# Kernel optimization log

Hardware: AMD Instinct MI355X
Metric: run time of the kernel (lower is better)

Reference implementation:

```python
import jax, jax.numpy as jnp
import numpy as np

EPS = 1e-8
NUM_HEADS = 4


def setup_inputs() -> dict:
    key = jax.random.key(0)
    ks = jax.random.split(key, 20)
    N, D = 8192, 200      # total nodes, gnn/text dim
    B = 4                  # graphs (text batch)
    E, DEG = 4096, 16      # hyperedges, nodes per hyperedge
    H = 128                # fusion hidden dim
    f = lambda k, s: jax.random.normal(k, s, dtype=jnp.float32) * 0.05
    return {
        "x": jax.random.normal(ks[0], (N, D), dtype=jnp.float32),
        "text": jax.random.normal(ks[1], (B, D), dtype=jnp.float32),
        "W": f(ks[2], (D, D)),
        "b": jnp.zeros((D,), jnp.float32),
        "gate_w": f(ks[3], (D, 1)),
        "gate_b": jnp.zeros((1,), jnp.float32),
        "gnn_w": f(ks[4], (D, H)), "gnn_b": f(ks[5], (H,)),
        "text_w": f(ks[6], (D, H)), "text_b": f(ks[7], (H,)),
        "in_w": f(ks[8], (H, 3 * H)), "in_b": f(ks[9], (3 * H,)),
        "attn_out_w": f(ks[10], (H, H)), "attn_out_b": f(ks[11], (H,)),
        "fgate_w": f(ks[12], (2 * H, H)), "fgate_b": f(ks[13], (H,)),
        "outp_w": f(ks[14], (H, D)), "outp_b": f(ks[15], (D,)),
        "edge_nodes": jax.random.randint(ks[16], (E, DEG), 0, N),
    }


def _forward(x, text, W, b, gate_w, gate_b, gnn_w, gnn_b, text_w, text_b,
             in_w, in_b, attn_out_w, attn_out_b, fgate_w, fgate_b,
             outp_w, outp_b, edge_nodes):
    N, D = x.shape
    E, DEG = edge_nodes.shape
    # --- HypergraphConv: incidence build + normalized Laplacian propagation ---
    out = x @ W                                         # [N, D]
    # H[node, edge] = 1/len(edge); duplicates overwrite (set), as in torch loop
    Hinc = jnp.zeros((N, E), x.dtype).at[edge_nodes, jnp.arange(E)[:, None]].set(1.0 / DEG)
    Dv = Hinc.sum(axis=1)                               # node degree [N]
    De = Hinc.sum(axis=0)                               # edge degree [E]
    dv = 1.0 / jnp.sqrt(Dv + EPS)
    de = 1.0 / (De + EPS)
    Hl = Hinc * dv[:, None]                             # Dv^-1/2 H
    L = (Hl * de[None, :]) @ Hl.T                       # Dv^-1/2 H De^-1 H^T Dv^-1/2
    hyper_out = L @ out                                 # [N, D]
    alpha = jax.nn.sigmoid(x.mean(axis=0, keepdims=True) @ gate_w + gate_b)  # [1,1]
    gnn_feat = alpha * out + (1.0 - alpha) * hyper_out + b
    # --- CrossModalAttentionFusion on per-graph node features (3D path) ---
    B = text.shape[0]
    Nn = N // B
    gnn3 = gnn_feat.reshape(B, Nn, D)
    gp = gnn3 @ gnn_w + gnn_b                           # [B, Nn, H]
    tp = (text @ text_w + text_b)[:, None, :]           # [B, 1, H]
    Hd = gp.shape[-1]
    hd = Hd // NUM_HEADS
    q = gp @ in_w[:, :Hd] + in_b[:Hd]
    k = tp @ in_w[:, Hd:2 * Hd] + in_b[Hd:2 * Hd]
    v = tp @ in_w[:, 2 * Hd:] + in_b[2 * Hd:]
    qh = q.reshape(B, Nn, NUM_HEADS, hd).transpose(0, 2, 1, 3)   # [B,h,Nn,hd]
    kh = k.reshape(B, 1, NUM_HEADS, hd).transpose(0, 2, 1, 3)    # [B,h,1,hd]
    vh = v.reshape(B, 1, NUM_HEADS, hd).transpose(0, 2, 1, 3)
    scores = jnp.einsum("bhqd,bhkd->bhqk", qh, kh) / jnp.sqrt(jnp.float32(hd))
    attn = jax.nn.softmax(scores, axis=-1)              # kv_len=1 -> ones
    att = jnp.einsum("bhqk,bhkd->bhqd", attn, vh)
    att = att.transpose(0, 2, 1, 3).reshape(B, Nn, Hd) @ attn_out_w + attn_out_b
    g = jax.nn.sigmoid(jnp.concatenate([gp, att], axis=-1) @ fgate_w + fgate_b)
    fused = g * gp + (1.0 - g) * att
    return fused @ outp_w + outp_b                      # [B, Nn, D]


def reference(x, text, W, b, gate_w, gate_b, gnn_w, gnn_b, text_w, text_b,
              in_w, in_b, attn_out_w, attn_out_b, fgate_w, fgate_b,
              outp_w, outp_b, edge_nodes):
    return _forward(x, text, W, b, gate_w, gate_b, gnn_w, gnn_b, text_w, text_b,
                    in_w, in_b, attn_out_w, attn_out_b, fgate_w, fgate_b,
                    outp_w, outp_b, edge_nodes)
```

## Files before the change

kernel.cpp:

```cpp
#include <hip/hip_runtime.h>
#include <hip/hip_bf16.h>

#define NODES 8192
#define DIM   200
#define NEDGE 4096
#define DEGREE 16
#define NB    4
#define NNODE 2048
#define HD    128
#define MT    8
#define ECAP  64

__global__ void k_front(const float* __restrict__ x, const int* __restrict__ en,
                        const float* __restrict__ W, const float* __restrict__ gnn_w,
                        const float* __restrict__ bias, const float* __restrict__ gnn_b,
                        const float* __restrict__ text, const float* __restrict__ text_w,
                        const float* __restrict__ text_b, const float* __restrict__ in_w,
                        const float* __restrict__ in_b, const float* __restrict__ aow,
                        const float* __restrict__ aob, const float* __restrict__ fgw,
                        const float* __restrict__ fgb, float* __restrict__ colsum,
                        int* __restrict__ cnt, int* __restrict__ emask,
                        float* __restrict__ Wg, float* __restrict__ bg,
                        float* __restrict__ attO, float* __restrict__ attg) {
    __shared__ float st[DIM];
    __shared__ float part[2][HD];
    __shared__ float vin[HD];
    int b = blockIdx.x, t = threadIdx.x;
    if (b < 256) {
        if (t < DIM) {
            float acc = 0.f;
            int r0 = b * 32;
            for (int r = 0; r < 32; r++) acc += x[(r0 + r) * DIM + t];
            atomicAdd(&colsum[t], acc);
        }
        return;
    }
    if (b < 272) {
        int e = (b - 256) * 256 + t;
        int idx[DEGREE];
#pragma unroll
        for (int i = 0; i < DEGREE; i++) idx[i] = en[e * DEGREE + i];
        int mask = 0;
#pragma unroll
        for (int i = 0; i < DEGREE; i++) {
            bool uniq = true;
            for (int j = 0; j < i; j++) uniq = uniq && (idx[j] != idx[i]);
            if (uniq) { mask |= (1 << i); atomicAdd(&cnt[idx[i]], 1); }
        }
        emask[e] = mask;
        return;
    }
    if (b < 372) {
        int r = 2 * (b - 272) + (t >> 7);
        int c = t & 127;
        const float* vec = &W[r * DIM];
        float acc = 0.f;
        for (int k = 0; k < DIM; k++) acc += vec[k] * gnn_w[k * HD + c];
        Wg[r * HD + c] = acc;
        return;
    }
    if (b == 372) {
        if (t < HD) {
            float acc = 0.f;
            for (int k = 0; k < DIM; k++) acc += bias[k] * gnn_w[k * HD + t];
            bg[t] = acc + gnn_b[t];
        }
        return;
    }
    int g = b - 373;
    int c = t & 127, h = t >> 7;
    if (t < DIM) st[t] = text[g * DIM + t];
    __syncthreads();
    {
        float acc = 0.f;
        int k0 = h * 100;
        for (int k = k0; k < k0 + 100; k++) acc += st[k] * text_w[k * HD + c];
        part[h][c] = acc;
    }
    __syncthreads();
    if (t < HD) vin[t] = part[0][t] + part[1][t] + text_b[t];
    __syncthreads();
    {
        float acc = 0.f;
        int k0 = h * 64;
        for (int k = k0; k < k0 + 64; k++) acc += vin[k] * in_w[k * 3 * HD + 2 * HD + c];
        part[h][c] = acc;
    }
    __syncthreads();
    if (t < HD) vin[t] = part[0][t] + part[1][t] + in_b[2 * HD + t];
    __syncthreads();
    {
        float acc = 0.f;
        int k0 = h * 64;
        for (int k = k0; k < k0 + 64; k++) acc += vin[k] * aow[k * HD + c];
        part[h][c] = acc;
    }
    __syncthreads();
    if (t < HD) {
        float ao = part[0][t] + part[1][t] + aob[t];
        attO[g * HD + t] = ao;
        vin[t] = ao;
    }
    __syncthreads();
    {
        float acc = 0.f;
        int k0 = h * 64;
        for (int k = k0; k < k0 + 64; k++) acc += vin[k] * fgw[(HD + k) * HD + c];
        part[h][c] = acc;
    }
    __syncthreads();
    if (t < HD) attg[g * HD + t] = part[0][t] + part[1][t] + fgb[t];
}

__global__ void k_mid(const float* __restrict__ colsum, const float* __restrict__ gate_w,
                      const float* __restrict__ gate_b, float* __restrict__ alpha,
                      const int* __restrict__ cnt, int* __restrict__ off,
                      int* __restrict__ cursor, float* __restrict__ dv) {
    __shared__ float redf[1024];
    __shared__ int wsum[16];
    int t = threadIdx.x;
    if (blockIdx.x == 0) {
        redf[t] = (t < DIM) ? colsum[t] * gate_w[t] : 0.f;
        __syncthreads();
        for (int o = 512; o > 0; o >>= 1) {
            if (t < o) redf[t] += redf[t + o];
            __syncthreads();
        }
        if (t == 0) {
            float z = redf[0] / (float)NODES + gate_b[0];
            alpha[0] = 1.0f / (1.0f + expf(-z));
        }
        return;
    }
    int base = t * 8;
    int local[8];
    int s = 0;
#pragma unroll
    for (int i = 0; i < 8; i++) { local[i] = cnt[base + i]; s += local[i]; }
    int lane = t & 63, wv = t >> 6;
    int v = s;
    for (int d = 1; d < 64; d <<= 1) {
        int u = __shfl_up(v, d);
        if (lane >= d) v += u;
    }
    if (lane == 63) wsum[wv] = v;
    __syncthreads();
    if (t == 0) {
        int run = 0;
        for (int i = 0; i < 16; i++) { int tmp = wsum[i]; wsum[i] = run; run += tmp; }
    }
    __syncthreads();
    int run = wsum[wv] + v - s;
#pragma unroll
    for (int i = 0; i < 8; i++) {
        off[base + i] = run;
        cursor[base + i] = run;
        dv[base + i] = 1.0f / sqrtf((float)local[i] * (1.0f / 16.0f) + 1e-8f);
        run += local[i];
    }
    if (t == 1023) off[NODES] = run;
}

__global__ void k_xwgfill(const float* __restrict__ x, const float* __restrict__ Wg,
                          float* __restrict__ out2, const int* __restrict__ en,
                          const int* __restrict__ emask, int* __restrict__ cursor,
                          int* __restrict__ elist) {
    __shared__ float sx[MT][DIM];
    int t = threadIdx.x;
    if (blockIdx.x >= NODES / MT) {
        int e = (blockIdx.x - NODES / MT) * 256 + t;
        int m = emask[e];
#pragma unroll
        for (int i = 0; i < DEGREE; i++) {
            if ((m >> i) & 1) {
                int n = en[e * DEGREE + i];
                int p = atomicAdd(&cursor[n], 1);
                elist[p] = e;
            }
        }
        return;
    }
    int bm = blockIdx.x * MT;
    for (int i = t; i < MT * DIM; i += 256) sx[i / DIM][i % DIM] = x[bm * DIM + i];
    __syncthreads();
    int c = t & 127, rg = t >> 7;
    float acc[4] = {0.f, 0.f, 0.f, 0.f};
    for (int k = 0; k < DIM; k++) {
        float w = Wg[k * HD + c];
#pragma unroll
        for (int i = 0; i < 4; i++) acc[i] += sx[rg * 4 + i][k] * w;
    }
#pragma unroll
    for (int i = 0; i < 4; i++) out2[(bm + rg * 4 + i) * HD + c] = acc[i];
}

__global__ void k_tE(const int* __restrict__ en, const int* __restrict__ emask,
                     const float* __restrict__ dv, const float* __restrict__ out2,
                     float* __restrict__ tE) {
    int e = blockIdx.x * 2 + (threadIdx.x >> 7);
    int c = threadIdx.x & 127;
    int m = emask[e];
    float De = (float)__popc(m) * (1.0f / 16.0f);
    float de = 1.0f / (De + 1e-8f);
    float acc = 0.f;
#pragma unroll
    for (int i = 0; i < DEGREE; i++) {
        if ((m >> i) & 1) {
            int nd = en[e * DEGREE + i];
            acc += dv[nd] * out2[nd * HD + c];
        }
    }
    tE[e * HD + c] = de * acc;
}

__global__ void k_tail(const float* __restrict__ out2, const float* __restrict__ tE,
                       const float* __restrict__ dv, const int* __restrict__ off,
                       const int* __restrict__ elist, const float* __restrict__ alpha,
                       const float* __restrict__ bg, const float* __restrict__ fgw,
                       const float* __restrict__ attO, const float* __restrict__ attg,
                       const float* __restrict__ opw, const float* __restrict__ opb,
                       float* __restrict__ out) {
    __shared__ float sgp[MT][HD];
    __shared__ int   sl[MT][ECAP];
    __shared__ int   scount[MT];
    int bm = blockIdx.x * MT;
    int b = bm >> 11;
    int t = threadIdx.x;
    {
        int r = t >> 5, l = t & 31;
        int n = bm + r;
        int j0 = off[n], j1 = off[n + 1];
        int cc = j1 - j0;
        if (l == 0) scount[r] = cc;
        int lim = cc < ECAP ? cc : ECAP;
        for (int j = l; j < lim; j += 32) sl[r][j] = elist[j0 + j];
    }
    __syncthreads();
    int c = t & 127, rg = t >> 7;
    float a = alpha[0];
    float bgc = bg[c];
#pragma unroll
    for (int i = 0; i < 4; i++) {
        int r = rg * 4 + i;
        int n = bm + r;
        int cc = scount[r];
        int lim = cc < ECAP ? cc : ECAP;
        float hyp = 0.f;
        for (int j = 0; j < lim; j++) hyp += tE[sl[r][j] * HD + c];
        if (cc > ECAP) {
            int j0 = off[n];
            for (int j = ECAP; j < cc; j++) hyp += tE[elist[j0 + j] * HD + c];
        }
        hyp *= dv[n] * (1.0f / 256.0f);
        sgp[r][c] = a * out2[n * HD + c] + (1.0f - a) * hyp + bgc;
    }
    __syncthreads();
    float ao = attO[b * HD + c];
    float ag = attg[b * HD + c];
    float acc[4] = {ag, ag, ag, ag};
    for (int j = 0; j < HD; j++) {
        float w = fgw[j * HD + c];
#pragma unroll
        for (int i = 0; i < 4; i++) acc[i] += sgp[rg * 4 + i][j] * w;
    }
    __syncthreads();
#pragma unroll
    for (int i = 0; i < 4; i++) {
        int r = rg * 4 + i;
        float g = 1.0f / (1.0f + expf(-acc[i]));
        sgp[r][c] = g * sgp[r][c] + (1.0f - g) * ao;
    }
    __syncthreads();
    if (t < DIM) {
        float accO[MT];
        float ob = opb[t];
#pragma unroll
        for (int i = 0; i < MT; i++) accO[i] = ob;
        for (int j = 0; j < HD; j++) {
            float w = opw[j * DIM + t];
#pragma unroll
            for (int i = 0; i < MT; i++) accO[i] += sgp[i][j] * w;
        }
#pragma unroll
        for (int i = 0; i < MT; i++) out[(bm + i) * DIM + t] = accO[i];
    }
}

extern "C" void kernel_launch(void* const* d_in, const int* in_sizes, int n_in,
                              void* d_out, int out_size, void* d_ws, size_t ws_size,
                              hipStream_t stream) {
    const float* x      = (const float*)d_in[0];
    const float* text   = (const float*)d_in[1];
    const float* W      = (const float*)d_in[2];
    const float* bias   = (const float*)d_in[3];
    const float* gate_w = (const float*)d_in[4];
    const float* gate_b = (const float*)d_in[5];
    const float* gnn_w  = (const float*)d_in[6];
    const float* gnn_b  = (const float*)d_in[7];
    const float* text_w = (const float*)d_in[8];
    const float* text_b = (const float*)d_in[9];
    const float* in_w   = (const float*)d_in[10];
    const float* in_b   = (const float*)d_in[11];
    const float* aow    = (const float*)d_in[12];
    const float* aob    = (const float*)d_in[13];
    const float* fgw    = (const float*)d_in[14];
    const float* fgb    = (const float*)d_in[15];
    const float* opw    = (const float*)d_in[16];
    const float* opb    = (const float*)d_in[17];
    const int*   en     = (const int*)d_in[18];
    float* out = (float*)d_out;

    char* p = (char*)d_ws;
    int*   cnt    = (int*)p;   p += NODES * sizeof(int);
    float* colsum = (float*)p; p += DIM * sizeof(float);
    float* out2   = (float*)p; p += (size_t)NODES * HD * sizeof(float);
    float* tE     = (float*)p; p += (size_t)NEDGE * HD * sizeof(float);
    float* Wg     = (float*)p; p += DIM * HD * sizeof(float);
    float* dv     = (float*)p; p += NODES * sizeof(float);
    float* alpha  = (float*)p; p += sizeof(float);
    float* bg     = (float*)p; p += HD * sizeof(float);
    float* attO   = (float*)p; p += NB * HD * sizeof(float);
    float* attg   = (float*)p; p += NB * HD * sizeof(float);
    int*   off    = (int*)p;   p += (NODES + 1) * sizeof(int);
    int*   cursor = (int*)p;   p += NODES * sizeof(int);
    int*   emask  = (int*)p;   p += NEDGE * sizeof(int);
    int*   elist  = (int*)p;   p += (size_t)NEDGE * DEGREE * sizeof(int);

    hipMemsetAsync(cnt, 0, (NODES + DIM) * sizeof(int), stream);

    k_front<<<377, 256, 0, stream>>>(x, en, W, gnn_w, bias, gnn_b, text, text_w,
                                     text_b, in_w, in_b, aow, aob, fgw, fgb,
                                     colsum, cnt, emask, Wg, bg, attO, attg);
    k_mid<<<2, 1024, 0, stream>>>(colsum, gate_w, gate_b, alpha, cnt, off, cursor, dv);
    k_xwgfill<<<NODES / MT + 16, 256, 0, stream>>>(x, Wg, out2, en, emask, cursor, elist);
    k_tE<<<NEDGE / 2, 256, 0, stream>>>(en, emask, dv, out2, tE);
    k_tail<<<NODES / MT, 256, 0, stream>>>(out2, tE, dv, off, elist, alpha, bg, fgw,
                                           attO, attg, opw, opb, out);
}
```

Measured before the change: 173.9 us.

## Replace CSR node-to-edge gather with atomic scatter from hyperedges

Drops the prefix-scan kernel and the CSR edge-list build. Each hyperedge block now computes its aggregated value and atomically adds it into a per-node accumulator, instead of the tail kernel gathering tE through the edge list. This removes one kernel launch, the per-node atomic cursor fill and the indirect gather. In exchange it adds a large memset of the accumulator, float atomics with nondeterministic summation order, and the dv computation is folded into the projection kernel as extra blocks. The x tile is now loaded into shared memory with float4.

```diff
diff --git a/kernel.cpp b/kernel.cpp
--- a/kernel.cpp
+++ b/kernel.cpp
@@ -9,7 +9,6 @@
 #define NNODE 2048
 #define HD    128
 #define MT    8
-#define ECAP  64
 
 __global__ void k_front(const float* __restrict__ x, const int* __restrict__ en,
                         const float* __restrict__ W, const float* __restrict__ gnn_w,
@@ -112,130 +111,79 @@
     if (t < HD) attg[g * HD + t] = part[0][t] + part[1][t] + fgb[t];
 }
 
-__global__ void k_mid(const float* __restrict__ colsum, const float* __restrict__ gate_w,
-                      const float* __restrict__ gate_b, float* __restrict__ alpha,
-                      const int* __restrict__ cnt, int* __restrict__ off,
-                      int* __restrict__ cursor, float* __restrict__ dv) {
-    __shared__ float redf[1024];
-    __shared__ int wsum[16];
+__global__ void k_xwg(const float* __restrict__ x, const float* __restrict__ Wg,
+                      float* __restrict__ out2, const float* __restrict__ colsum,
+                      const float* __restrict__ gate_w, const float* __restrict__ gate_b,
+                      float* __restrict__ alpha, const int* __restrict__ cnt,
+                      float* __restrict__ dv) {
+    __shared__ float sx[MT * DIM];
     int t = threadIdx.x;
-    if (blockIdx.x == 0) {
-        redf[t] = (t < DIM) ? colsum[t] * gate_w[t] : 0.f;
+    if (blockIdx.x == NODES / MT) {
+        __shared__ float red[256];
+        red[t] = (t < DIM) ? colsum[t] * gate_w[t] : 0.f;
         __syncthreads();
-        for (int o = 512; o > 0; o >>= 1) {
-            if (t < o) redf[t] += redf[t + o];
+        for (int o = 128; o > 0; o >>= 1) {
+            if (t < o) red[t] += red[t + o];
             __syncthreads();
         }
         if (t == 0) {
-            float z = redf[0] / (float)NODES + gate_b[0];
+            float z = red[0] / (float)NODES + gate_b[0];
             alpha[0] = 1.0f / (1.0f + expf(-z));
         }
         return;
     }
-    int base = t * 8;
-    int local[8];
-    int s = 0;
-#pragma unroll
-    for (int i = 0; i < 8; i++) { local[i] = cnt[base + i]; s += local[i]; }
-    int lane = t & 63, wv = t >> 6;
-    int v = s;
-    for (int d = 1; d < 64; d <<= 1) {
-        int u = __shfl_up(v, d);
-        if (lane >= d) v += u;
-    }
-    if (lane == 63) wsum[wv] = v;
-    __syncthreads();
-    if (t == 0) {
-        int run = 0;
-        for (int i = 0; i < 16; i++) { int tmp = wsum[i]; wsum[i] = run; run += tmp; }
-    }
-    __syncthreads();
-    int run = wsum[wv] + v - s;
-#pragma unroll
-    for (int i = 0; i < 8; i++) {
-        off[base + i] = run;
-        cursor[base + i] = run;
-        dv[base + i] = 1.0f / sqrtf((float)local[i] * (1.0f / 16.0f) + 1e-8f);
-        run += local[i];
-    }
-    if (t == 1023) off[NODES] = run;
-}
-
-__global__ void k_xwgfill(const float* __restrict__ x, const float* __restrict__ Wg,
-                          float* __restrict__ out2, const int* __restrict__ en,
-                          const int* __restrict__ emask, int* __restrict__ cursor,
-                          int* __restrict__ elist) {
-    __shared__ float sx[MT][DIM];
-    int t = threadIdx.x;
-    if (blockIdx.x >= NODES / MT) {
-        int e = (blockIdx.x - NODES / MT) * 256 + t;
-        int m = emask[e];
-#pragma unroll
-        for (int i = 0; i < DEGREE; i++) {
-            if ((m >> i) & 1) {
-                int n = en[e * DEGREE + i];
-                int p = atomicAdd(&cursor[n], 1);
-                elist[p] = e;
-            }
-        }
+    if (blockIdx.x > NODES / MT) {
+        int n = (blockIdx.x - NODES / MT - 1) * 256 + t;
+        dv[n] = 1.0f / sqrtf((float)cnt[n] * (1.0f / 16.0f) + 1e-8f);
         return;
     }
     int bm = blockIdx.x * MT;
-    for (int i = t; i < MT * DIM; i += 256) sx[i / DIM][i % DIM] = x[bm * DIM + i];
+    const float4* x4 = (const float4*)(x + bm * DIM);
+    float4* sx4 = (float4*)sx;
+    for (int i = t; i < MT * DIM / 4; i += 256) sx4[i] = x4[i];
     __syncthreads();
     int c = t & 127, rg = t >> 7;
     float acc[4] = {0.f, 0.f, 0.f, 0.f};
     for (int k = 0; k < DIM; k++) {
         float w = Wg[k * HD + c];
 #pragma unroll
-        for (int i = 0; i < 4; i++) acc[i] += sx[rg * 4 + i][k] * w;
+        for (int i = 0; i < 4; i++) acc[i] += sx[(rg * 4 + i) * DIM + k] * w;
     }
 #pragma unroll
     for (int i = 0; i < 4; i++) out2[(bm + rg * 4 + i) * HD + c] = acc[i];
 }
 
-__global__ void k_tE(const int* __restrict__ en, const int* __restrict__ emask,
-                     const float* __restrict__ dv, const float* __restrict__ out2,
-                     float* __restrict__ tE) {
+__global__ void k_edge(const int* __restrict__ en, const int* __restrict__ emask,
+                       const float* __restrict__ dv, const float* __restrict__ out2,
+                       float* __restrict__ accum) {
     int e = blockIdx.x * 2 + (threadIdx.x >> 7);
     int c = threadIdx.x & 127;
     int m = emask[e];
     float De = (float)__popc(m) * (1.0f / 16.0f);
     float de = 1.0f / (De + 1e-8f);
+    int nd[DEGREE];
+#pragma unroll
+    for (int i = 0; i < DEGREE; i++) nd[i] = en[e * DEGREE + i];
     float acc = 0.f;
 #pragma unroll
-    for (int i = 0; i < DEGREE; i++) {
-        if ((m >> i) & 1) {
-            int nd = en[e * DEGREE + i];
-            acc += dv[nd] * out2[nd * HD + c];
-        }
-    }
-    tE[e * HD + c] = de * acc;
-}
-
-__global__ void k_tail(const float* __restrict__ out2, const float* __restrict__ tE,
-                       const float* __restrict__ dv, const int* __restrict__ off,
-                       const int* __restrict__ elist, const float* __restrict__ alpha,
+    for (int i = 0; i < DEGREE; i++)
+        if ((m >> i) & 1) acc += dv[nd[i]] * out2[nd[i] * HD + c];
+    float s = de * acc;
+#pragma unroll
+    for (int i = 0; i < DEGREE; i++)
+        if ((m >> i) & 1) atomicAdd(&accum[nd[i] * HD + c], s);
+}
+
+__global__ void k_tail(const float* __restrict__ out2, const float* __restrict__ accum,
+                       const float* __restrict__ dv, const float* __restrict__ alpha,
                        const float* __restrict__ bg, const float* __restrict__ fgw,
                        const float* __restrict__ attO, const float* __restrict__ attg,
                        const float* __restrict__ opw, const float* __restrict__ opb,
                        float* __restrict__ out) {
     __shared__ float sgp[MT][HD];
-    __shared__ int   sl[MT][ECAP];
-    __shared__ int   scount[MT];
     int bm = blockIdx.x * MT;
     int b = bm >> 11;
     int t = threadIdx.x;
-    {
-        int r = t >> 5, l = t & 31;
-        int n = bm + r;
-        int j0 = off[n], j1 = off[n + 1];
-        int cc = j1 - j0;
-        if (l == 0) scount[r] = cc;
-        int lim = cc < ECAP ? cc : ECAP;
-        for (int j = l; j < lim; j += 32) sl[r][j] = elist[j0 + j];
-    }
-    __syncthreads();
     int c = t & 127, rg = t >> 7;
     float a = alpha[0];
     float bgc = bg[c];
@@ -243,15 +191,7 @@
     for (int i = 0; i < 4; i++) {
         int r = rg * 4 + i;
         int n = bm + r;
-        int cc = scount[r];
-        int lim = cc < ECAP ? cc : ECAP;
-        float hyp = 0.f;
-        for (int j = 0; j < lim; j++) hyp += tE[sl[r][j] * HD + c];
-        if (cc > ECAP) {
-            int j0 = off[n];
-            for (int j = ECAP; j < cc; j++) hyp += tE[elist[j0 + j] * HD + c];
-        }
-        hyp *= dv[n] * (1.0f / 256.0f);
+        float hyp = accum[n * HD + c] * dv[n] * (1.0f / 256.0f);
         sgp[r][c] = a * out2[n * HD + c] + (1.0f - a) * hyp + bgc;
     }
     __syncthreads();
@@ -313,27 +253,24 @@
     char* p = (char*)d_ws;
     int*   cnt    = (int*)p;   p += NODES * sizeof(int);
     float* colsum = (float*)p; p += DIM * sizeof(float);
+    float* accum  = (float*)p; p += (size_t)NODES * HD * sizeof(float);
     float* out2   = (float*)p; p += (size_t)NODES * HD * sizeof(float);
-    float* tE     = (float*)p; p += (size_t)NEDGE * HD * sizeof(float);
     float* Wg     = (float*)p; p += DIM * HD * sizeof(float);
     float* dv     = (float*)p; p += NODES * sizeof(float);
     float* alpha  = (float*)p; p += sizeof(float);
     float* bg     = (float*)p; p += HD * sizeof(float);
     float* attO   = (float*)p; p += NB * HD * sizeof(float);
     float* attg   = (float*)p; p += NB * HD * sizeof(float);
-    int*   off    = (int*)p;   p += (NODES + 1) * sizeof(int);
-    int*   cursor = (int*)p;   p += NODES * sizeof(int);
     int*   emask  = (int*)p;   p += NEDGE * sizeof(int);
-    int*   elist  = (int*)p;   p += (size_t)NEDGE * DEGREE * sizeof(int);
-
-    hipMemsetAsync(cnt, 0, (NODES + DIM) * sizeof(int), stream);
+
+    hipMemsetAsync(cnt, 0, (NODES + DIM + NODES * HD) * sizeof(int), stream);
 
     k_front<<<377, 256, 0, stream>>>(x, en, W, gnn_w, bias, gnn_b, text, text_w,
                                      text_b, in_w, in_b, aow, aob, fgw, fgb,
                                      colsum, cnt, emask, Wg, bg, attO, attg);
-    k_mid<<<2, 1024, 0, stream>>>(colsum, gate_w, gate_b, alpha, cnt, off, cursor, dv);
-    k_xwgfill<<<NODES / MT + 16, 256, 0, stream>>>(x, Wg, out2, en, emask, cursor, elist);
-    k_tE<<<NEDGE / 2, 256, 0, stream>>>(en, emask, dv, out2, tE);
-    k_tail<<<NODES / MT, 256, 0, stream>>>(out2, tE, dv, off, elist, alpha, bg, fgw,
+    k_xwg<<<NODES / MT + 1 + NODES / 256, 256, 0, stream>>>(x, Wg, out2, colsum, gate_w,
+                                                            gate_b, alpha, cnt, dv);
+    k_edge<<<NEDGE / 2, 256, 0, stream>>>(en, emask, dv, out2, accum);
+    k_tail<<<NODES / MT, 256, 0, stream>>>(out2, accum, dv, alpha, bg, fgw,
                                            attO, attg, opw, opb, out);
 }
```

Measured after the change: 185.4 us. 6.6% more time.
